# Performance work log

Hardware: AMD Instinct MI355X
Metric: run time of the kernel (lower is better)

The kernel has to match this reference:

```python
import jax, jax.numpy as jnp
import numpy as np

B = 65536
IN_DIM = 512
H0, H1 = 256, 128
HEAD_H = 64
D = 12
K_MAX = 3
EPS = 1e-5
# predecessor indices per disease (topologically ordered DAG)
PRED_LISTS = [[], [0], [0], [1, 2], [0, 3], [2], [4, 5], [1, 6], [3, 7], [6, 8], [5, 9], [8, 10, 9]]


def setup_inputs() -> dict:
    key = jax.random.key(0)
    ks = jax.random.split(key, 16)
    x = jax.random.normal(ks[0], (B, IN_DIM), jnp.float32)
    enc_W0 = jax.random.normal(ks[1], (IN_DIM, H0), jnp.float32) * 0.04
    enc_b0 = jnp.zeros((H0,), jnp.float32)
    bn0_g = jnp.ones((H0,), jnp.float32)
    bn0_b = jnp.zeros((H0,), jnp.float32)
    bn0_m = jax.random.normal(ks[2], (H0,), jnp.float32) * 0.1
    bn0_v = jax.random.uniform(ks[3], (H0,), jnp.float32, 0.5, 1.5)
    enc_W1 = jax.random.normal(ks[4], (H0, H1), jnp.float32) * 0.06
    enc_b1 = jnp.zeros((H1,), jnp.float32)
    bn1_g = jnp.ones((H1,), jnp.float32)
    bn1_b = jnp.zeros((H1,), jnp.float32)
    bn1_m = jax.random.normal(ks[5], (H1,), jnp.float32) * 0.1
    bn1_v = jax.random.uniform(ks[6], (H1,), jnp.float32, 0.5, 1.5)
    w_init = jax.random.normal(ks[7], (D, H1), jnp.float32) * 0.09   # head.layer1 (pass-1 logit)
    b_init = jnp.zeros((D,), jnp.float32)
    Wz = jax.random.normal(ks[8], (D, H1, HEAD_H), jnp.float32) * 0.09   # head first layer, z-columns
    Wp = jax.random.normal(ks[9], (D, K_MAX, HEAD_H), jnp.float32) * 0.09  # head first layer, predecessor columns (padded)
    bh = jnp.zeros((D, HEAD_H), jnp.float32)
    Wo = jax.random.normal(ks[10], (D, HEAD_H), jnp.float32) * 0.12
    bo = jnp.zeros((D,), jnp.float32)
    idx = np.zeros((D, K_MAX), np.int32)
    w = np.zeros((D, K_MAX), np.float32)
    for d, preds in enumerate(PRED_LISTS):
        for j, p in enumerate(preds):
            idx[d, j] = p
            w[d, j] = 0.5  # DAG edge weight; zero entries are padding
    return {"x": x, "enc_W0": enc_W0, "enc_b0": enc_b0, "bn0_g": bn0_g, "bn0_b": bn0_b,
            "bn0_m": bn0_m, "bn0_v": bn0_v, "enc_W1": enc_W1, "enc_b1": enc_b1,
            "bn1_g": bn1_g, "bn1_b": bn1_b, "bn1_m": bn1_m, "bn1_v": bn1_v,
            "w_init": w_init, "b_init": b_init, "Wz": Wz, "Wp": Wp, "bh": bh,
            "Wo": Wo, "bo": bo, "pred_w": jnp.asarray(w), "pred_idx": jnp.asarray(idx)}


def reference(x, enc_W0, enc_b0, bn0_g, bn0_b, bn0_m, bn0_v, enc_W1, enc_b1,
              bn1_g, bn1_b, bn1_m, bn1_v, w_init, b_init, Wz, Wp, bh, Wo, bo,
              pred_w, pred_idx):
    # Shared encoder: Linear -> BatchNorm(eval stats) -> ReLU, twice (dropout identity at eval)
    h = x @ enc_W0 + enc_b0
    h = jax.nn.relu((h - bn0_m) * jax.lax.rsqrt(bn0_v + EPS) * bn0_g + bn0_b)
    z = h @ enc_W1 + enc_b1
    z = jax.nn.relu((z - bn1_m) * jax.lax.rsqrt(bn1_v + EPS) * bn1_g + bn1_b)  # [B, H1]
    # Pass 1: initial per-disease prediction = sigmoid(head.layer1(z))
    p = jax.nn.sigmoid(z @ w_init.T + b_init)  # [B, D]
    # Pass 2: DAG gather of predecessor predictions, edge-weighted; padding slots have weight 0
    aug = p[:, pred_idx] * pred_w  # [B, D, K_MAX]
    # Per-disease head: Linear(H1 + k -> HEAD_H) split into z-part + predecessor-part, ReLU, Linear(HEAD_H -> 1), sigmoid
    hid = jax.nn.relu(jnp.einsum('be,deh->bdh', z, Wz) + jnp.einsum('bdk,dkh->bdh', aug, Wp) + bh)
    out = jax.nn.sigmoid(jnp.einsum('bdh,dh->bd', hid, Wo) + bo)  # [B, D] = torch.cat of final_preds
    return out
```

## Files before the change

kernel.cpp:

```cpp
#include <hip/hip_runtime.h>
#include <stdint.h>

#define B_TOT   65536
#define IN_DIM  512
#define H0      256
#define H1      128
#define HH      64
#define NDIS    12

#define BM      64
#define NBLK    (B_TOT / BM)

typedef __bf16 bf16_t;
typedef __bf16 bf16x4 __attribute__((ext_vector_type(4)));
typedef __bf16 bf16x8 __attribute__((ext_vector_type(8)));
typedef float  f32x4  __attribute__((ext_vector_type(4)));

#define WS_W0T   0u
#define WS_W1T   262144u
#define WS_WZT   327680u
#define WS_WIT   524288u
#define WS_AL0   528384u
#define WS_BE0   529408u
#define WS_AL1   530432u
#define WS_BE1   530944u
#define WS_NEED  531456u

#define L_PS     17408u
#define L_PART   22528u
#define L_TOTAL  49152u

__device__ __forceinline__ f32x4 MF(bf16x8 a, bf16x8 b, f32x4 c) {
    return __builtin_amdgcn_mfma_f32_16x16x32_bf16(a, b, c, 0, 0, 0);
}
__device__ __forceinline__ void dma16(const void* g, void* l) {
    __builtin_amdgcn_global_load_lds(
        (const __attribute__((address_space(1))) unsigned*)g,
        (__attribute__((address_space(3))) unsigned*)l, 16, 0, 0);
}
__device__ __forceinline__ void BAR() {
    asm volatile("s_waitcnt lgkmcnt(0)\ns_barrier" ::: "memory");
}
#define WAITBAR(N) asm volatile("s_waitcnt vmcnt(" #N ") lgkmcnt(0)\ns_barrier" ::: "memory")

#define PACK8(o, lo, hi) { o[0]=(bf16_t)lo[0]; o[1]=(bf16_t)lo[1]; o[2]=(bf16_t)lo[2]; o[3]=(bf16_t)lo[3]; \
                           o[4]=(bf16_t)hi[0]; o[5]=(bf16_t)hi[1]; o[6]=(bf16_t)hi[2]; o[7]=(bf16_t)hi[3]; }

__global__ void prep_kernel(const float* __restrict__ W0, const float* __restrict__ b0,
                            const float* __restrict__ g0, const float* __restrict__ bb0,
                            const float* __restrict__ mm0, const float* __restrict__ vv0,
                            const float* __restrict__ W1, const float* __restrict__ b1,
                            const float* __restrict__ g1, const float* __restrict__ bb1,
                            const float* __restrict__ mm1, const float* __restrict__ vv1,
                            const float* __restrict__ w_init, const float* __restrict__ Wz,
                            char* __restrict__ ws)
{
    bf16_t* W0t = (bf16_t*)(ws + WS_W0T);
    bf16_t* W1t = (bf16_t*)(ws + WS_W1T);
    bf16_t* Wzt = (bf16_t*)(ws + WS_WZT);
    bf16_t* wiT = (bf16_t*)(ws + WS_WIT);
    float* al0 = (float*)(ws + WS_AL0);
    float* be0 = (float*)(ws + WS_BE0);
    float* al1 = (float*)(ws + WS_AL1);
    float* be1 = (float*)(ws + WS_BE1);

    int t = blockIdx.x * 256 + threadIdx.x;

    {
        int c = t >> 9, k = t & 511;
        W0t[t] = (bf16_t)W0[k * H0 + c];
    }
    if (t < H1 * H0) {
        int c = t >> 8, k = t & 255;
        W1t[t] = (bf16_t)W1[k * H1 + c];
    }
    if (t < NDIS * HH * H1) {
        int d = t >> 13, r = t & 8191, h = r >> 7, e = r & 127;
        Wzt[t] = (bf16_t)Wz[d * 8192 + e * 64 + h];
    }
    if (t < 16 * H1) {
        int d = t >> 7, e = t & 127;
        wiT[t] = (d < NDIS) ? (bf16_t)w_init[d * H1 + e] : (bf16_t)0.0f;
    }
    if (t < H0) {
        float a = g0[t] * rsqrtf(vv0[t] + 1e-5f);
        al0[t] = a;
        be0[t] = (b0[t] - mm0[t]) * a + bb0[t];
    }
    if (t < H1) {
        float a = g1[t] * rsqrtf(vv1[t] + 1e-5f);
        al1[t] = a;
        be1[t] = (b1[t] - mm1[t]) * a + bb1[t];
    }
}

__global__ __launch_bounds__(256, 3) void fused_kernel(
    const float* __restrict__ x,
    const bf16_t* __restrict__ W0t, const bf16_t* __restrict__ W1t,
    const float* __restrict__ al0, const float* __restrict__ be0,
    const float* __restrict__ al1, const float* __restrict__ be1,
    const bf16_t* __restrict__ Wzt, const bf16_t* __restrict__ wiT,
    const float* __restrict__ b_init, const float* __restrict__ Wp,
    const float* __restrict__ bh, const float* __restrict__ Wo,
    const float* __restrict__ bo, const float* __restrict__ pred_w,
    const int* __restrict__ pred_idx, float* __restrict__ out)
{
    __shared__ __align__(16) char smem[L_TOTAL];

    const int tid  = threadIdx.x;
    const int lane = tid & 63, w = tid >> 6;
    const int l15 = lane & 15, lg = lane >> 4;
    const int m0 = blockIdx.x * BM;

    const float* xsrc[4];
    float* xdst[4];
    #pragma unroll
    for (int i = 0; i < 4; ++i) {
        int row = w * 16 + i * 4 + (lane >> 4);
        int gslot = (lane & 15) ^ (row & 15);
        xsrc[i] = x + (size_t)(m0 + row) * IN_DIM + gslot * 4;
        xdst[i] = (float*)smem + (w * 16 + i * 4) * 64;
    }
    const bf16_t* wg = W0t + (size_t)(w * 64 + l15) * IN_DIM + lg * 8;

    f32x4 acc[4][4] = {};
    bf16x8 aA[2][4], aB[2][4];

#define ISSUE_DMA(K) { _Pragma("unroll") \
    for (int i = 0; i < 4; ++i) dma16(xsrc[i] + (K) * 64, xdst[i] + ((K) % 3) * 4096); }
#define ISSUE_A(K, SET) { _Pragma("unroll") \
    for (int mf = 0; mf < 4; ++mf) { \
        SET[0][mf] = *(const bf16x8*)(wg + (size_t)mf * 16 * IN_DIM + (K) * 64); \
        SET[1][mf] = *(const bf16x8*)(wg + (size_t)mf * 16 * IN_DIM + (K) * 64 + 32); } }
#define MFMA_STEP(K, CUR) { \
    const float* xb = (const float*)smem + ((K) % 3) * 1024 * 4; \
    __builtin_amdgcn_s_setprio(1); \
    _Pragma("unroll") \
    for (int kf = 0; kf < 2; ++kf) { \
        _Pragma("unroll") \
        for (int nf = 0; nf < 4; ++nf) { \
            int s0 = kf * 8 + lg * 2; \
            f32x4 u = *(const f32x4*)(xb + (nf * 16 + l15) * 64 + ((s0    ) ^ l15) * 4); \
            f32x4 v = *(const f32x4*)(xb + (nf * 16 + l15) * 64 + ((s0 + 1) ^ l15) * 4); \
            bf16x8 b; PACK8(b, u, v); \
            _Pragma("unroll") \
            for (int mf = 0; mf < 4; ++mf) acc[mf][nf] = MF(CUR[kf][mf], b, acc[mf][nf]); \
        } \
    } \
    __builtin_amdgcn_s_setprio(0); }

    ISSUE_DMA(0);
    ISSUE_A(0, aA);
    ISSUE_DMA(1);

    WAITBAR(12); ISSUE_DMA(2); ISSUE_A(1, aB); MFMA_STEP(0, aA);
    WAITBAR(12); ISSUE_DMA(3); ISSUE_A(2, aA); MFMA_STEP(1, aB);
    WAITBAR(12); ISSUE_DMA(4); ISSUE_A(3, aB); MFMA_STEP(2, aA);
    WAITBAR(12); ISSUE_DMA(5); ISSUE_A(4, aA); MFMA_STEP(3, aB);
    WAITBAR(12); ISSUE_DMA(6); ISSUE_A(5, aB); MFMA_STEP(4, aA);
    WAITBAR(12); ISSUE_DMA(7); ISSUE_A(6, aA); MFMA_STEP(5, aB);
    WAITBAR(12);               ISSUE_A(7, aB); MFMA_STEP(6, aA);
    WAITBAR(8);                                MFMA_STEP(7, aB);

    asm volatile("s_waitcnt vmcnt(0) lgkmcnt(0)\ns_barrier" ::: "memory");

    {
        bf16_t* hs = (bf16_t*)smem;
        #pragma unroll
        for (int mf = 0; mf < 4; ++mf) {
            int c = w * 64 + mf * 16 + lg * 4;
            f32x4 al = *(const f32x4*)(al0 + c);
            f32x4 be = *(const f32x4*)(be0 + c);
            #pragma unroll
            for (int nf = 0; nf < 4; ++nf) {
                int r = nf * 16 + l15;
                bf16x4 o;
                #pragma unroll
                for (int j = 0; j < 4; ++j)
                    o[j] = (bf16_t)fmaxf(acc[mf][nf][j] * al[j] + be[j], 0.f);
                *(bf16x4*)(hs + r * 264 + c) = o;
            }
        }
    }
    BAR();

    f32x4 acc2[2][4] = {};
    {
        const bf16_t* hs  = (const bf16_t*)smem;
        const bf16_t* w1g = W1t + (size_t)(w * 32 + l15) * H0 + lg * 8;
        bf16x8 aP[2], aQ[2];
        aP[0] = *(const bf16x8*)(w1g);
        aP[1] = *(const bf16x8*)(w1g + 16 * H0);
        aQ[0] = *(const bf16x8*)(w1g + 32);
        aQ[1] = *(const bf16x8*)(w1g + 16 * H0 + 32);
        #pragma unroll
        for (int kf = 0; kf < 8; ++kf) {
            bf16x8 ac0 = (kf & 1) ? aQ[0] : aP[0];
            bf16x8 ac1 = (kf & 1) ? aQ[1] : aP[1];
            if (kf < 6) {
                if (kf & 1) {
                    aQ[0] = *(const bf16x8*)(w1g + (kf + 2) * 32);
                    aQ[1] = *(const bf16x8*)(w1g + 16 * H0 + (kf + 2) * 32);
                } else {
                    aP[0] = *(const bf16x8*)(w1g + (kf + 2) * 32);
                    aP[1] = *(const bf16x8*)(w1g + 16 * H0 + (kf + 2) * 32);
                }
            }
            #pragma unroll
            for (int nf = 0; nf < 4; ++nf) {
                bf16x8 b = *(const bf16x8*)(hs + (nf * 16 + l15) * 264 + kf * 32 + lg * 8);
                acc2[0][nf] = MF(ac0, b, acc2[0][nf]);
                acc2[1][nf] = MF(ac1, b, acc2[1][nf]);
            }
        }
    }
    BAR();
    {
        bf16_t* zs = (bf16_t*)smem;
        #pragma unroll
        for (int mf = 0; mf < 2; ++mf) {
            int c = w * 32 + mf * 16 + lg * 4;
            f32x4 al = *(const f32x4*)(al1 + c);
            f32x4 be = *(const f32x4*)(be1 + c);
            #pragma unroll
            for (int nf = 0; nf < 4; ++nf) {
                int r = nf * 16 + l15;
                bf16x4 o;
                #pragma unroll
                for (int j = 0; j < 4; ++j)
                    o[j] = (bf16_t)fmaxf(acc2[mf][nf][j] * al[j] + be[j], 0.f);
                *(bf16x4*)(zs + r * 136 + c) = o;
            }
        }
    }
    BAR();

    const bf16_t* zs = (const bf16_t*)smem;
    float* psf  = (float*)(smem + L_PS);
    float* part = (float*)(smem + L_PART);
    const bf16_t* wzg = Wzt + (size_t)(w * 16 + l15) * H1 + lg * 8;
    const int hb = w * 16 + lg * 4;

    bf16x8 az0 = *(const bf16x8*)(wzg);
    bf16x8 az1 = *(const bf16x8*)(wzg + 32);
    bf16x8 az2 = *(const bf16x8*)(wzg + 64);
    bf16x8 az3 = *(const bf16x8*)(wzg + 96);
    int   ci0 = pred_idx[0], ci1 = pred_idx[1], ci2 = pred_idx[2];
    float cq0 = pred_w[0],  cq1 = pred_w[1],  cq2 = pred_w[2];
    f32x4 cbh = *(const f32x4*)(bh + hb);
    f32x4 cwo = *(const f32x4*)(Wo + hb);
    f32x4 cpa = *(const f32x4*)(Wp + hb);
    f32x4 cpb = *(const f32x4*)(Wp + 64 + hb);
    f32x4 cpc = *(const f32x4*)(Wp + 128 + hb);

    {
        f32x4 pacc = {};
        #pragma unroll
        for (int kf = 0; kf < 4; ++kf) {
            bf16x8 aw = *(const bf16x8*)(wiT + l15 * H1 + kf * 32 + lg * 8);
            bf16x8 bz = *(const bf16x8*)(zs + (w * 16 + l15) * 136 + kf * 32 + lg * 8);
            pacc = MF(aw, bz, pacc);
        }
        f32x4 pv;
        #pragma unroll
        for (int j = 0; j < 4; ++j) {
            int d = lg * 4 + j;
            float bi = (d < NDIS) ? b_init[d] : 0.f;
            pv[j] = 1.f / (1.f + __expf(-(pacc[j] + bi)));
        }
        *(f32x4*)(psf + (w * 16 + l15) * 20 + lg * 4) = pv;
    }
    BAR();

    #pragma unroll 1
    for (int d = 0; d < NDIS; ++d) {
        bf16x8 an0 = az0, an1 = az1, an2 = az2, an3 = az3;
        int   ni0 = ci0, ni1 = ci1, ni2 = ci2;
        float nq0 = cq0, nq1 = cq1, nq2 = cq2;
        f32x4 nbh = cbh, nwo = cwo, npa = cpa, npb = cpb, npc = cpc;
        if (d < NDIS - 1) {
            const bf16_t* p = wzg + (size_t)(d + 1) * 8192;
            an0 = *(const bf16x8*)(p);      an1 = *(const bf16x8*)(p + 32);
            an2 = *(const bf16x8*)(p + 64); an3 = *(const bf16x8*)(p + 96);
            ni0 = pred_idx[(d + 1) * 3]; ni1 = pred_idx[(d + 1) * 3 + 1]; ni2 = pred_idx[(d + 1) * 3 + 2];
            nq0 = pred_w[(d + 1) * 3];   nq1 = pred_w[(d + 1) * 3 + 1];   nq2 = pred_w[(d + 1) * 3 + 2];
            nbh = *(const f32x4*)(bh + (d + 1) * 64 + hb);
            nwo = *(const f32x4*)(Wo + (d + 1) * 64 + hb);
            npa = *(const f32x4*)(Wp + (d + 1) * 192 + hb);
            npb = *(const f32x4*)(Wp + (d + 1) * 192 + 64 + hb);
            npc = *(const f32x4*)(Wp + (d + 1) * 192 + 128 + hb);
        }

        #pragma unroll
        for (int nf = 0; nf < 4; ++nf) {
            const bf16_t* zr = zs + (nf * 16 + l15) * 136 + lg * 8;
            f32x4 hacc = {};
            hacc = MF(az0, *(const bf16x8*)(zr),      hacc);
            hacc = MF(az1, *(const bf16x8*)(zr + 32), hacc);
            hacc = MF(az2, *(const bf16x8*)(zr + 64), hacc);
            hacc = MF(az3, *(const bf16x8*)(zr + 96), hacc);
            int r = nf * 16 + l15;
            float a0 = psf[r * 20 + ci0] * cq0;
            float a1 = psf[r * 20 + ci1] * cq1;
            float a2 = psf[r * 20 + ci2] * cq2;
            float s = 0.f;
            #pragma unroll
            for (int j = 0; j < 4; ++j) {
                float v = hacc[j] + cbh[j] + a0 * cpa[j] + a1 * cpb[j] + a2 * cpc[j];
                s += fmaxf(v, 0.f) * cwo[j];
            }
            s += __shfl_xor(s, 16);
            s += __shfl_xor(s, 32);
            if (lane < 16) part[d * 256 + r * 4 + w] = s;
        }
        az0 = an0; az1 = an1; az2 = an2; az3 = an3;
        ci0 = ni0; ci1 = ni1; ci2 = ni2;
        cq0 = nq0; cq1 = nq1; cq2 = nq2;
        cbh = nbh; cwo = nwo; cpa = npa; cpb = npb; cpc = npc;
    }
    BAR();

    {
        float* obuf = (float*)(smem + L_PS);
        #pragma unroll
        for (int i = 0; i < 3; ++i) {
            int e = tid * 3 + i;
            int d = e % 12, r = e / 12;
            f32x4 p = *(const f32x4*)(part + d * 256 + r * 4);
            float s = p[0] + p[1] + p[2] + p[3] + bo[d];
            obuf[e] = 1.f / (1.f + __expf(-s));
        }
    }
    BAR();
    if (tid < 192) {
        f32x4 o = *(const f32x4*)((const float*)(smem + L_PS) + tid * 4);
        *(f32x4*)(out + (size_t)blockIdx.x * 768 + tid * 4) = o;
    }
}

extern "C" void kernel_launch(void* const* d_in, const int* in_sizes, int n_in,
                              void* d_out, int out_size, void* d_ws, size_t ws_size,
                              hipStream_t stream) {
    if (ws_size < (size_t)WS_NEED) return;

    const float* x      = (const float*)d_in[0];
    const float* W0     = (const float*)d_in[1];
    const float* b0     = (const float*)d_in[2];
    const float* g0     = (const float*)d_in[3];
    const float* bb0    = (const float*)d_in[4];
    const float* mm0    = (const float*)d_in[5];
    const float* vv0    = (const float*)d_in[6];
    const float* W1     = (const float*)d_in[7];
    const float* b1     = (const float*)d_in[8];
    const float* g1     = (const float*)d_in[9];
    const float* bb1    = (const float*)d_in[10];
    const float* mm1    = (const float*)d_in[11];
    const float* vv1    = (const float*)d_in[12];
    const float* w_init = (const float*)d_in[13];
    const float* b_init = (const float*)d_in[14];
    const float* Wz     = (const float*)d_in[15];
    const float* Wp     = (const float*)d_in[16];
    const float* bh     = (const float*)d_in[17];
    const float* Wo     = (const float*)d_in[18];
    const float* bo     = (const float*)d_in[19];
    const float* pred_w = (const float*)d_in[20];
    const int*   pred_idx = (const int*)d_in[21];

    char* ws = (char*)d_ws;
    const bf16_t* W0t = (const bf16_t*)(ws + WS_W0T);
    const bf16_t* W1t = (const bf16_t*)(ws + WS_W1T);
    const bf16_t* Wzt = (const bf16_t*)(ws + WS_WZT);
    const bf16_t* wiT = (const bf16_t*)(ws + WS_WIT);
    const float* al0 = (const float*)(ws + WS_AL0);
    const float* be0 = (const float*)(ws + WS_BE0);
    const float* al1 = (const float*)(ws + WS_AL1);
    const float* be1 = (const float*)(ws + WS_BE1);

    prep_kernel<<<dim3(512), dim3(256), 0, stream>>>(
        W0, b0, g0, bb0, mm0, vv0, W1, b1, g1, bb1, mm1, vv1, w_init, Wz, ws);

    fused_kernel<<<dim3(NBLK), dim3(256), 0, stream>>>(
        x, W0t, W1t, al0, be0, al1, be1, Wzt, wiT, b_init, Wp, bh, Wo, bo,
        pred_w, pred_idx, (float*)d_out);
}
```

Measured before the change: 95.94 us.

## Split fused kernel into encoder and head kernels with z staged in global bf16

Splits the single fused kernel into an encoder kernel that writes z as bf16 to a workspace buffer and a separate head kernel that DMAs it back into LDS. The encoder now loads x through registers, converts it to bf16 before storing a double-buffered swizzled LDS tile, and replaces the triple-buffered fp32 async DMA pipeline. Smaller LDS footprints allow a 4-blocks-per-CU launch bound. The cost is an extra 16 MB global round trip for z plus an additional kernel launch, and the register-staged x loads may expose more latency than the async DMA did.

```diff
diff --git a/kernel.cpp b/kernel.cpp
--- a/kernel.cpp
+++ b/kernel.cpp
@@ -24,11 +24,8 @@
 #define WS_BE0   529408u
 #define WS_AL1   530432u
 #define WS_BE1   530944u
-#define WS_NEED  531456u
-
-#define L_PS     17408u
-#define L_PART   22528u
-#define L_TOTAL  49152u
+#define WS_Z     531456u
+#define WS_NEED  (531456u + 16777216u)
 
 __device__ __forceinline__ f32x4 MF(bf16x8 a, bf16x8 b, f32x4 c) {
     return __builtin_amdgcn_mfma_f32_16x16x32_bf16(a, b, c, 0, 0, 0);
@@ -41,7 +38,6 @@
 __device__ __forceinline__ void BAR() {
     asm volatile("s_waitcnt lgkmcnt(0)\ns_barrier" ::: "memory");
 }
-#define WAITBAR(N) asm volatile("s_waitcnt vmcnt(" #N ") lgkmcnt(0)\ns_barrier" ::: "memory")
 
 #define PACK8(o, lo, hi) { o[0]=(bf16_t)lo[0]; o[1]=(bf16_t)lo[1]; o[2]=(bf16_t)lo[2]; o[3]=(bf16_t)lo[3]; \
                            o[4]=(bf16_t)hi[0]; o[5]=(bf16_t)hi[1]; o[6]=(bf16_t)hi[2]; o[7]=(bf16_t)hi[3]; }
@@ -94,75 +90,88 @@
     }
 }
 
-__global__ __launch_bounds__(256, 3) void fused_kernel(
+__global__ __launch_bounds__(256, 4) void enc_kernel(
     const float* __restrict__ x,
     const bf16_t* __restrict__ W0t, const bf16_t* __restrict__ W1t,
     const float* __restrict__ al0, const float* __restrict__ be0,
     const float* __restrict__ al1, const float* __restrict__ be1,
-    const bf16_t* __restrict__ Wzt, const bf16_t* __restrict__ wiT,
-    const float* __restrict__ b_init, const float* __restrict__ Wp,
-    const float* __restrict__ bh, const float* __restrict__ Wo,
-    const float* __restrict__ bo, const float* __restrict__ pred_w,
-    const int* __restrict__ pred_idx, float* __restrict__ out)
+    bf16_t* __restrict__ zg)
 {
-    __shared__ __align__(16) char smem[L_TOTAL];
+    __shared__ __align__(16) char smem[33792];
 
     const int tid  = threadIdx.x;
     const int lane = tid & 63, w = tid >> 6;
     const int l15 = lane & 15, lg = lane >> 4;
     const int m0 = blockIdx.x * BM;
 
-    const float* xsrc[4];
-    float* xdst[4];
+    bf16_t* xs = (bf16_t*)smem;
+
+    const int r0 = tid >> 3, s0 = tid & 7;
+    const float* sgp0 = x + (size_t)(m0 + r0) * IN_DIM + s0 * 8;
+    const float* sgp1 = x + (size_t)(m0 + r0 + 32) * IN_DIM + s0 * 8;
+    const int sd0 = r0 * 64 + ((s0 ^ (r0 & 7)) << 3);
+    const int sd1 = (r0 + 32) * 64 + ((s0 ^ ((r0 + 32) & 7)) << 3);
+
+    const bf16_t* wg = W0t + (size_t)(w * 64 + l15) * IN_DIM + lg * 8;
+    const int xb0 = ((lg ^ (l15 & 7)) << 3);
+    const int xb1 = (((4 | lg) ^ (l15 & 7)) << 3);
+
+    f32x4 acc[4][4] = {};
+    f32x4 lo0, hi0, lo1, hi1;
+    bf16x8 aS0[4], aS1[4];
+
+    lo0 = *(const f32x4*)(sgp0);     hi0 = *(const f32x4*)(sgp0 + 4);
+    lo1 = *(const f32x4*)(sgp1);     hi1 = *(const f32x4*)(sgp1 + 4);
+    { bf16x8 o; PACK8(o, lo0, hi0); *(bf16x8*)(xs + sd0) = o; }
+    { bf16x8 o; PACK8(o, lo1, hi1); *(bf16x8*)(xs + sd1) = o; }
+    lo0 = *(const f32x4*)(sgp0 + 64); hi0 = *(const f32x4*)(sgp0 + 68);
+    lo1 = *(const f32x4*)(sgp1 + 64); hi1 = *(const f32x4*)(sgp1 + 68);
     #pragma unroll
-    for (int i = 0; i < 4; ++i) {
-        int row = w * 16 + i * 4 + (lane >> 4);
-        int gslot = (lane & 15) ^ (row & 15);
-        xsrc[i] = x + (size_t)(m0 + row) * IN_DIM + gslot * 4;
-        xdst[i] = (float*)smem + (w * 16 + i * 4) * 64;
-    }
-    const bf16_t* wg = W0t + (size_t)(w * 64 + l15) * IN_DIM + lg * 8;
-
-    f32x4 acc[4][4] = {};
-    bf16x8 aA[2][4], aB[2][4];
-
-#define ISSUE_DMA(K) { _Pragma("unroll") \
-    for (int i = 0; i < 4; ++i) dma16(xsrc[i] + (K) * 64, xdst[i] + ((K) % 3) * 4096); }
-#define ISSUE_A(K, SET) { _Pragma("unroll") \
-    for (int mf = 0; mf < 4; ++mf) { \
-        SET[0][mf] = *(const bf16x8*)(wg + (size_t)mf * 16 * IN_DIM + (K) * 64); \
-        SET[1][mf] = *(const bf16x8*)(wg + (size_t)mf * 16 * IN_DIM + (K) * 64 + 32); } }
-#define MFMA_STEP(K, CUR) { \
-    const float* xb = (const float*)smem + ((K) % 3) * 1024 * 4; \
-    __builtin_amdgcn_s_setprio(1); \
-    _Pragma("unroll") \
-    for (int kf = 0; kf < 2; ++kf) { \
-        _Pragma("unroll") \
-        for (int nf = 0; nf < 4; ++nf) { \
-            int s0 = kf * 8 + lg * 2; \
-            f32x4 u = *(const f32x4*)(xb + (nf * 16 + l15) * 64 + ((s0    ) ^ l15) * 4); \
-            f32x4 v = *(const f32x4*)(xb + (nf * 16 + l15) * 64 + ((s0 + 1) ^ l15) * 4); \
-            bf16x8 b; PACK8(b, u, v); \
-            _Pragma("unroll") \
-            for (int mf = 0; mf < 4; ++mf) acc[mf][nf] = MF(CUR[kf][mf], b, acc[mf][nf]); \
-        } \
-    } \
-    __builtin_amdgcn_s_setprio(0); }
-
-    ISSUE_DMA(0);
-    ISSUE_A(0, aA);
-    ISSUE_DMA(1);
-
-    WAITBAR(12); ISSUE_DMA(2); ISSUE_A(1, aB); MFMA_STEP(0, aA);
-    WAITBAR(12); ISSUE_DMA(3); ISSUE_A(2, aA); MFMA_STEP(1, aB);
-    WAITBAR(12); ISSUE_DMA(4); ISSUE_A(3, aB); MFMA_STEP(2, aA);
-    WAITBAR(12); ISSUE_DMA(5); ISSUE_A(4, aA); MFMA_STEP(3, aB);
-    WAITBAR(12); ISSUE_DMA(6); ISSUE_A(5, aB); MFMA_STEP(4, aA);
-    WAITBAR(12); ISSUE_DMA(7); ISSUE_A(6, aA); MFMA_STEP(5, aB);
-    WAITBAR(12);               ISSUE_A(7, aB); MFMA_STEP(6, aA);
-    WAITBAR(8);                                MFMA_STEP(7, aB);
-
-    asm volatile("s_waitcnt vmcnt(0) lgkmcnt(0)\ns_barrier" ::: "memory");
+    for (int mf = 0; mf < 4; ++mf) {
+        aS0[mf] = *(const bf16x8*)(wg + (size_t)mf * 16 * IN_DIM);
+        aS1[mf] = *(const bf16x8*)(wg + (size_t)mf * 16 * IN_DIM + 32);
+    }
+    BAR();
+
+    #pragma unroll 1
+    for (int ks = 0; ks < 8; ++ks) {
+        if (ks < 7) {
+            bf16_t* xw = xs + ((ks + 1) & 1) * 4096;
+            { bf16x8 o; PACK8(o, lo0, hi0); *(bf16x8*)(xw + sd0) = o; }
+            { bf16x8 o; PACK8(o, lo1, hi1); *(bf16x8*)(xw + sd1) = o; }
+            if (ks < 6) {
+                lo0 = *(const f32x4*)(sgp0 + (ks + 2) * 64); hi0 = *(const f32x4*)(sgp0 + (ks + 2) * 64 + 4);
+                lo1 = *(const f32x4*)(sgp1 + (ks + 2) * 64); hi1 = *(const f32x4*)(sgp1 + (ks + 2) * 64 + 4);
+            }
+        }
+        __builtin_amdgcn_sched_barrier(0);
+
+        const bf16_t* xr = xs + (ks & 1) * 4096;
+        __builtin_amdgcn_s_setprio(1);
+        #pragma unroll
+        for (int nf = 0; nf < 4; ++nf) {
+            bf16x8 b = *(const bf16x8*)(xr + nf * 1024 + l15 * 64 + xb0);
+            #pragma unroll
+            for (int mf = 0; mf < 4; ++mf) acc[mf][nf] = MF(aS0[mf], b, acc[mf][nf]);
+        }
+        #pragma unroll
+        for (int nf = 0; nf < 4; ++nf) {
+            bf16x8 b = *(const bf16x8*)(xr + nf * 1024 + l15 * 64 + xb1);
+            #pragma unroll
+            for (int mf = 0; mf < 4; ++mf) acc[mf][nf] = MF(aS1[mf], b, acc[mf][nf]);
+        }
+        __builtin_amdgcn_s_setprio(0);
+
+        if (ks < 7) {
+            #pragma unroll
+            for (int mf = 0; mf < 4; ++mf) {
+                aS0[mf] = *(const bf16x8*)(wg + (size_t)mf * 16 * IN_DIM + (ks + 1) * 64);
+                aS1[mf] = *(const bf16x8*)(wg + (size_t)mf * 16 * IN_DIM + (ks + 1) * 64 + 32);
+            }
+        }
+        __builtin_amdgcn_sched_barrier(0);
+        BAR();
+    }
 
     {
         bf16_t* hs = (bf16_t*)smem;
@@ -184,10 +193,10 @@
     }
     BAR();
 
-    f32x4 acc2[2][4] = {};
     {
         const bf16_t* hs  = (const bf16_t*)smem;
         const bf16_t* w1g = W1t + (size_t)(w * 32 + l15) * H0 + lg * 8;
+        f32x4 acc2[2][4] = {};
         bf16x8 aP[2], aQ[2];
         aP[0] = *(const bf16x8*)(w1g);
         aP[1] = *(const bf16x8*)(w1g + 16 * H0);
@@ -213,10 +222,6 @@
                 acc2[1][nf] = MF(ac1, b, acc2[1][nf]);
             }
         }
-    }
-    BAR();
-    {
-        bf16_t* zs = (bf16_t*)smem;
         #pragma unroll
         for (int mf = 0; mf < 2; ++mf) {
             int c = w * 32 + mf * 16 + lg * 4;
@@ -229,15 +234,42 @@
                 #pragma unroll
                 for (int j = 0; j < 4; ++j)
                     o[j] = (bf16_t)fmaxf(acc2[mf][nf][j] * al[j] + be[j], 0.f);
-                *(bf16x4*)(zs + r * 136 + c) = o;
-            }
-        }
-    }
-    BAR();
+                *(bf16x4*)(zg + (size_t)(m0 + r) * H1 + c) = o;
+            }
+        }
+    }
+}
+
+#define HL_PS    16384u
+#define HL_PART  21504u
+#define HL_TOTAL 33792u
+
+__global__ __launch_bounds__(256, 4) void head_kernel(
+    const bf16_t* __restrict__ zg,
+    const bf16_t* __restrict__ Wzt, const bf16_t* __restrict__ wiT,
+    const float* __restrict__ b_init, const float* __restrict__ Wp,
+    const float* __restrict__ bh, const float* __restrict__ Wo,
+    const float* __restrict__ bo, const float* __restrict__ pred_w,
+    const int* __restrict__ pred_idx, float* __restrict__ out)
+{
+    __shared__ __align__(16) char smem[HL_TOTAL];
+
+    const int tid  = threadIdx.x;
+    const int lane = tid & 63, w = tid >> 6;
+    const int l15 = lane & 15, lg = lane >> 4;
+    const int m0 = blockIdx.x * BM;
+
+    {
+        const char* zsrc = (const char*)zg + (size_t)blockIdx.x * 16384 + w * 4096;
+        char* zdst = smem + w * 4096;
+        #pragma unroll
+        for (int i = 0; i < 4; ++i)
+            dma16(zsrc + i * 1024 + lane * 16, zdst + i * 1024);
+    }
 
     const bf16_t* zs = (const bf16_t*)smem;
-    float* psf  = (float*)(smem + L_PS);
-    float* part = (float*)(smem + L_PART);
+    float* psf  = (float*)(smem + HL_PS);
+    float* part = (float*)(smem + HL_PART);
     const bf16_t* wzg = Wzt + (size_t)(w * 16 + l15) * H1 + lg * 8;
     const int hb = w * 16 + lg * 4;
 
@@ -253,12 +285,14 @@
     f32x4 cpb = *(const f32x4*)(Wp + 64 + hb);
     f32x4 cpc = *(const f32x4*)(Wp + 128 + hb);
 
+    asm volatile("s_waitcnt vmcnt(0) lgkmcnt(0)\ns_barrier" ::: "memory");
+
     {
         f32x4 pacc = {};
         #pragma unroll
         for (int kf = 0; kf < 4; ++kf) {
             bf16x8 aw = *(const bf16x8*)(wiT + l15 * H1 + kf * 32 + lg * 8);
-            bf16x8 bz = *(const bf16x8*)(zs + (w * 16 + l15) * 136 + kf * 32 + lg * 8);
+            bf16x8 bz = *(const bf16x8*)(zs + (w * 16 + l15) * H1 + kf * 32 + lg * 8);
             pacc = MF(aw, bz, pacc);
         }
         f32x4 pv;
@@ -290,10 +324,11 @@
             npb = *(const f32x4*)(Wp + (d + 1) * 192 + 64 + hb);
             npc = *(const f32x4*)(Wp + (d + 1) * 192 + 128 + hb);
         }
+        __builtin_amdgcn_sched_barrier(0);
 
         #pragma unroll
         for (int nf = 0; nf < 4; ++nf) {
-            const bf16_t* zr = zs + (nf * 16 + l15) * 136 + lg * 8;
+            const bf16_t* zr = zs + (nf * 16 + l15) * H1 + lg * 8;
             f32x4 hacc = {};
             hacc = MF(az0, *(const bf16x8*)(zr),      hacc);
             hacc = MF(az1, *(const bf16x8*)(zr + 32), hacc);
@@ -321,7 +356,7 @@
     BAR();
 
     {
-        float* obuf = (float*)(smem + L_PS);
+        float* obuf = (float*)(smem + HL_PS);
         #pragma unroll
         for (int i = 0; i < 3; ++i) {
             int e = tid * 3 + i;
@@ -333,7 +368,7 @@
     }
     BAR();
     if (tid < 192) {
-        f32x4 o = *(const f32x4*)((const float*)(smem + L_PS) + tid * 4);
+        f32x4 o = *(const f32x4*)((const float*)(smem + HL_PS) + tid * 4);
         *(f32x4*)(out + (size_t)blockIdx.x * 768 + tid * 4) = o;
     }
 }
@@ -375,11 +410,14 @@
     const float* be0 = (const float*)(ws + WS_BE0);
     const float* al1 = (const float*)(ws + WS_AL1);
     const float* be1 = (const float*)(ws + WS_BE1);
+    bf16_t* zg = (bf16_t*)(ws + WS_Z);
 
     prep_kernel<<<dim3(512), dim3(256), 0, stream>>>(
         W0, b0, g0, bb0, mm0, vv0, W1, b1, g1, bb1, mm1, vv1, w_init, Wz, ws);
 
-    fused_kernel<<<dim3(NBLK), dim3(256), 0, stream>>>(
-        x, W0t, W1t, al0, be0, al1, be1, Wzt, wiT, b_init, Wp, bh, Wo, bo,
-        pred_w, pred_idx, (float*)d_out);
-}
+    enc_kernel<<<dim3(NBLK), dim3(256), 0, stream>>>(
+        x, W0t, W1t, al0, be0, al1, be1, zg);
+
+    head_kernel<<<dim3(NBLK), dim3(256), 0, stream>>>(
+        zg, Wzt, wiT, b_init, Wp, bh, Wo, bo, pred_w, pred_idx, (float*)d_out);
+}
```

New measurement: 121.0 us. 1.26x slower.

## Stage x as bf16 in LDS via register loads instead of fp32 DMA ring

Applied to the files above, without the earlier changes.

Replaces the three-slot fp32 global_load_lds ring for x with register-staged loads. Each half of K is converted to bf16 once and written into a swizzled 32 KB LDS tile, so the MFMA loop reads bf16 fragments directly instead of packing fp32 per fragment. It also prefetches W1 and w_init fragments earlier, gives z its own LDS region to drop two barriers, and adds sched_barriers. LDS use grows to about 67 KB and launch bounds drop from 3 to 2 blocks per CU, trading occupancy for fewer barriers and conversions.

```diff
diff --git a/kernel.cpp b/kernel.cpp
--- a/kernel.cpp
+++ b/kernel.cpp
@@ -26,22 +26,18 @@
 #define WS_BE1   530944u
 #define WS_NEED  531456u
 
-#define L_PS     17408u
-#define L_PART   22528u
-#define L_TOTAL  49152u
+#define L_ZS     33792u
+#define L_PS     51200u
+#define L_PART   56320u
+#define L_TOTAL  68608u
 
 __device__ __forceinline__ f32x4 MF(bf16x8 a, bf16x8 b, f32x4 c) {
     return __builtin_amdgcn_mfma_f32_16x16x32_bf16(a, b, c, 0, 0, 0);
 }
-__device__ __forceinline__ void dma16(const void* g, void* l) {
-    __builtin_amdgcn_global_load_lds(
-        (const __attribute__((address_space(1))) unsigned*)g,
-        (__attribute__((address_space(3))) unsigned*)l, 16, 0, 0);
-}
 __device__ __forceinline__ void BAR() {
     asm volatile("s_waitcnt lgkmcnt(0)\ns_barrier" ::: "memory");
 }
-#define WAITBAR(N) asm volatile("s_waitcnt vmcnt(" #N ") lgkmcnt(0)\ns_barrier" ::: "memory")
+#define SB() __builtin_amdgcn_sched_barrier(0)
 
 #define PACK8(o, lo, hi) { o[0]=(bf16_t)lo[0]; o[1]=(bf16_t)lo[1]; o[2]=(bf16_t)lo[2]; o[3]=(bf16_t)lo[3]; \
                            o[4]=(bf16_t)hi[0]; o[5]=(bf16_t)hi[1]; o[6]=(bf16_t)hi[2]; o[7]=(bf16_t)hi[3]; }
@@ -94,7 +90,7 @@
     }
 }
 
-__global__ __launch_bounds__(256, 3) void fused_kernel(
+__global__ __launch_bounds__(256, 2) void fused_kernel(
     const float* __restrict__ x,
     const bf16_t* __restrict__ W0t, const bf16_t* __restrict__ W1t,
     const float* __restrict__ al0, const float* __restrict__ be0,
@@ -112,57 +108,63 @@
     const int l15 = lane & 15, lg = lane >> 4;
     const int m0 = blockIdx.x * BM;
 
-    const float* xsrc[4];
-    float* xdst[4];
-    #pragma unroll
-    for (int i = 0; i < 4; ++i) {
-        int row = w * 16 + i * 4 + (lane >> 4);
-        int gslot = (lane & 15) ^ (row & 15);
-        xsrc[i] = x + (size_t)(m0 + row) * IN_DIM + gslot * 4;
-        xdst[i] = (float*)smem + (w * 16 + i * 4) * 64;
-    }
+    const int srow = tid >> 2, squad = tid & 3;
+    const float* sgp = x + (size_t)(m0 + srow) * IN_DIM;
+    bf16_t* const xw = (bf16_t*)smem;
+    const bf16_t* const xr = (const bf16_t*)smem;
     const bf16_t* wg = W0t + (size_t)(w * 64 + l15) * IN_DIM + lg * 8;
 
+    f32x4 sv[16];
     f32x4 acc[4][4] = {};
-    bf16x8 aA[2][4], aB[2][4];
-
-#define ISSUE_DMA(K) { _Pragma("unroll") \
-    for (int i = 0; i < 4; ++i) dma16(xsrc[i] + (K) * 64, xdst[i] + ((K) % 3) * 4096); }
-#define ISSUE_A(K, SET) { _Pragma("unroll") \
-    for (int mf = 0; mf < 4; ++mf) { \
-        SET[0][mf] = *(const bf16x8*)(wg + (size_t)mf * 16 * IN_DIM + (K) * 64); \
-        SET[1][mf] = *(const bf16x8*)(wg + (size_t)mf * 16 * IN_DIM + (K) * 64 + 32); } }
-#define MFMA_STEP(K, CUR) { \
-    const float* xb = (const float*)smem + ((K) % 3) * 1024 * 4; \
-    __builtin_amdgcn_s_setprio(1); \
-    _Pragma("unroll") \
-    for (int kf = 0; kf < 2; ++kf) { \
-        _Pragma("unroll") \
-        for (int nf = 0; nf < 4; ++nf) { \
-            int s0 = kf * 8 + lg * 2; \
-            f32x4 u = *(const f32x4*)(xb + (nf * 16 + l15) * 64 + ((s0    ) ^ l15) * 4); \
-            f32x4 v = *(const f32x4*)(xb + (nf * 16 + l15) * 64 + ((s0 + 1) ^ l15) * 4); \
-            bf16x8 b; PACK8(b, u, v); \
-            _Pragma("unroll") \
-            for (int mf = 0; mf < 4; ++mf) acc[mf][nf] = MF(CUR[kf][mf], b, acc[mf][nf]); \
-        } \
-    } \
-    __builtin_amdgcn_s_setprio(0); }
-
-    ISSUE_DMA(0);
-    ISSUE_A(0, aA);
-    ISSUE_DMA(1);
-
-    WAITBAR(12); ISSUE_DMA(2); ISSUE_A(1, aB); MFMA_STEP(0, aA);
-    WAITBAR(12); ISSUE_DMA(3); ISSUE_A(2, aA); MFMA_STEP(1, aB);
-    WAITBAR(12); ISSUE_DMA(4); ISSUE_A(3, aB); MFMA_STEP(2, aA);
-    WAITBAR(12); ISSUE_DMA(5); ISSUE_A(4, aA); MFMA_STEP(3, aB);
-    WAITBAR(12); ISSUE_DMA(6); ISSUE_A(5, aB); MFMA_STEP(4, aA);
-    WAITBAR(12); ISSUE_DMA(7); ISSUE_A(6, aA); MFMA_STEP(5, aB);
-    WAITBAR(12);               ISSUE_A(7, aB); MFMA_STEP(6, aA);
-    WAITBAR(8);                                MFMA_STEP(7, aB);
-
-    asm volatile("s_waitcnt vmcnt(0) lgkmcnt(0)\ns_barrier" ::: "memory");
+    bf16x8 aA[8], aB[8];
+
+#define STAGE_ISSUE(hf) { _Pragma("unroll") for (int i = 0; i < 8; ++i) { \
+    int c = squad + i * 4; \
+    sv[2*i]   = *(const f32x4*)(sgp + (hf) * 256 + c * 8); \
+    sv[2*i+1] = *(const f32x4*)(sgp + (hf) * 256 + c * 8 + 4); } }
+#define STAGE_WRITE() { _Pragma("unroll") for (int i = 0; i < 8; ++i) { \
+    int c = squad + i * 4; int p = c ^ (srow & 31); \
+    bf16x8 o; PACK8(o, sv[2*i], sv[2*i+1]); \
+    *(bf16x8*)(xw + srow * 256 + p * 8) = o; } }
+#define ISSUE_A0(gk, SET) { _Pragma("unroll") for (int mf = 0; mf < 4; ++mf) { \
+    SET[mf]     = *(const bf16x8*)(wg + (size_t)mf * 16 * IN_DIM + (gk)); \
+    SET[mf + 4] = *(const bf16x8*)(wg + (size_t)mf * 16 * IN_DIM + (gk) + 32); } }
+#define G0_STEP(st, SET) { \
+    _Pragma("unroll") for (int kf = 0; kf < 2; ++kf) \
+    _Pragma("unroll") for (int nf = 0; nf < 4; ++nf) { \
+        int c = (st) * 8 + kf * 4 + lg; \
+        int p = c ^ (((nf & 1) << 4) | l15); \
+        bf16x8 b = *(const bf16x8*)(xr + (nf * 16 + l15) * 256 + p * 8); \
+        _Pragma("unroll") for (int mf = 0; mf < 4; ++mf) \
+            acc[mf][nf] = MF(SET[kf * 4 + mf], b, acc[mf][nf]); } }
+
+    STAGE_ISSUE(0); SB();
+    ISSUE_A0(0, aA); SB();
+    STAGE_WRITE();
+    BAR();
+
+    STAGE_ISSUE(1); SB();
+
+    ISSUE_A0(64,  aB); SB(); G0_STEP(0, aA); SB();
+    ISSUE_A0(128, aA); SB(); G0_STEP(1, aB); SB();
+    ISSUE_A0(192, aB); SB(); G0_STEP(2, aA); SB();
+    ISSUE_A0(256, aA); SB(); G0_STEP(3, aB);
+    BAR();
+    STAGE_WRITE();
+    BAR();
+
+    ISSUE_A0(320, aB); SB(); G0_STEP(0, aA); SB();
+    ISSUE_A0(384, aA); SB(); G0_STEP(1, aB); SB();
+    ISSUE_A0(448, aB); SB(); G0_STEP(2, aA); SB();
+    const bf16_t* w1g = W1t + (size_t)(w * 32 + l15) * H0 + lg * 8;
+    bf16x8 aP[2], aQ[2];
+    aP[0] = *(const bf16x8*)(w1g);
+    aP[1] = *(const bf16x8*)(w1g + 16 * H0);
+    aQ[0] = *(const bf16x8*)(w1g + 32);
+    aQ[1] = *(const bf16x8*)(w1g + 16 * H0 + 32);
+    SB();
+    G0_STEP(3, aB);
+    BAR();
 
     {
         bf16_t* hs = (bf16_t*)smem;
@@ -184,15 +186,10 @@
     }
     BAR();
 
-    f32x4 acc2[2][4] = {};
-    {
-        const bf16_t* hs  = (const bf16_t*)smem;
-        const bf16_t* w1g = W1t + (size_t)(w * 32 + l15) * H0 + lg * 8;
-        bf16x8 aP[2], aQ[2];
-        aP[0] = *(const bf16x8*)(w1g);
-        aP[1] = *(const bf16x8*)(w1g + 16 * H0);
-        aQ[0] = *(const bf16x8*)(w1g + 32);
-        aQ[1] = *(const bf16x8*)(w1g + 16 * H0 + 32);
+    {
+        const bf16_t* hs = (const bf16_t*)smem;
+        bf16_t* zs = (bf16_t*)(smem + L_ZS);
+        f32x4 acc2[2][4] = {};
         #pragma unroll
         for (int kf = 0; kf < 8; ++kf) {
             bf16x8 ac0 = (kf & 1) ? aQ[0] : aP[0];
@@ -213,10 +210,6 @@
                 acc2[1][nf] = MF(ac1, b, acc2[1][nf]);
             }
         }
-    }
-    BAR();
-    {
-        bf16_t* zs = (bf16_t*)smem;
         #pragma unroll
         for (int mf = 0; mf < 2; ++mf) {
             int c = w * 32 + mf * 16 + lg * 4;
@@ -233,14 +226,17 @@
             }
         }
     }
-    BAR();
-
-    const bf16_t* zs = (const bf16_t*)smem;
+
+    const bf16_t* zs = (const bf16_t*)(smem + L_ZS);
     float* psf  = (float*)(smem + L_PS);
     float* part = (float*)(smem + L_PART);
     const bf16_t* wzg = Wzt + (size_t)(w * 16 + l15) * H1 + lg * 8;
     const int hb = w * 16 + lg * 4;
 
+    bf16x8 wi0 = *(const bf16x8*)(wiT + l15 * H1 + lg * 8);
+    bf16x8 wi1 = *(const bf16x8*)(wiT + l15 * H1 + 32 + lg * 8);
+    bf16x8 wi2 = *(const bf16x8*)(wiT + l15 * H1 + 64 + lg * 8);
+    bf16x8 wi3 = *(const bf16x8*)(wiT + l15 * H1 + 96 + lg * 8);
     bf16x8 az0 = *(const bf16x8*)(wzg);
     bf16x8 az1 = *(const bf16x8*)(wzg + 32);
     bf16x8 az2 = *(const bf16x8*)(wzg + 64);
@@ -252,15 +248,16 @@
     f32x4 cpa = *(const f32x4*)(Wp + hb);
     f32x4 cpb = *(const f32x4*)(Wp + 64 + hb);
     f32x4 cpc = *(const f32x4*)(Wp + 128 + hb);
-
-    {
+    SB();
+    BAR();
+
+    {
+        const bf16_t* bz = zs + (w * 16 + l15) * 136 + lg * 8;
         f32x4 pacc = {};
-        #pragma unroll
-        for (int kf = 0; kf < 4; ++kf) {
-            bf16x8 aw = *(const bf16x8*)(wiT + l15 * H1 + kf * 32 + lg * 8);
-            bf16x8 bz = *(const bf16x8*)(zs + (w * 16 + l15) * 136 + kf * 32 + lg * 8);
-            pacc = MF(aw, bz, pacc);
-        }
+        pacc = MF(wi0, *(const bf16x8*)(bz),      pacc);
+        pacc = MF(wi1, *(const bf16x8*)(bz + 32), pacc);
+        pacc = MF(wi2, *(const bf16x8*)(bz + 64), pacc);
+        pacc = MF(wi3, *(const bf16x8*)(bz + 96), pacc);
         f32x4 pv;
         #pragma unroll
         for (int j = 0; j < 4; ++j) {
@@ -290,6 +287,7 @@
             npb = *(const f32x4*)(Wp + (d + 1) * 192 + 64 + hb);
             npc = *(const f32x4*)(Wp + (d + 1) * 192 + 128 + hb);
         }
+        SB();
 
         #pragma unroll
         for (int nf = 0; nf < 4; ++nf) {
```

After: 93.44 us. 1.03x faster.
